# Optimization experiments

Measured on AMD Instinct MI355X. Metric: run time of the kernel, lower is better.

Reference implementation:

```python
import jax, jax.numpy as jnp
import numpy as np

NUM_BITS = 4
BLOCK = 64
OUT_F, IN_F = 4096, 4096
RANK = 16


def _uniform_table():
    # BlockQuantizer.create_uniform_map(symmetric=False, num_bits=4)
    return jnp.linspace(-1.0, 1.0, 2 ** NUM_BITS).astype(jnp.float32)


def _dequantize(qweight, weight_max):
    """Unpack 4-bit codes (2 per byte), lookup codebook, apply per-64 block scale.
    qweight: [OUT*IN/2, 1] int32 in [0,256); weight_max: [OUT*IN/64, 1] float32.
    Returns [OUT_F, IN_F] float32."""
    table = _uniform_table()
    q = qweight[:, 0]
    idx_lo = q & 15          # packed at shift 0
    idx_hi = (q >> 4) & 15   # packed at shift 4
    w = jnp.stack([table[idx_lo], table[idx_hi]], axis=-1)  # [N/2, 2]
    w = w.reshape(-1, BLOCK) * weight_max                   # per-block scale
    return w.reshape(OUT_F, IN_F)


def setup_inputs() -> dict:
    key = jax.random.key(0)
    k1, k2, k3, k4, k5, k6 = jax.random.split(key, 6)
    x = jax.random.normal(k1, (4, 2048, IN_F), dtype=jnp.float32)
    qweight = jax.random.randint(k2, (OUT_F * IN_F // 2, 1), 0, 256, dtype=jnp.int32)
    weight_max = jax.random.uniform(k3, (OUT_F * IN_F // BLOCK, 1), dtype=jnp.float32,
                                    minval=0.01, maxval=1.0)
    lora_A = jax.random.normal(k4, (RANK, IN_F), dtype=jnp.float32) * 0.02
    lora_B = jax.random.normal(k5, (OUT_F, RANK), dtype=jnp.float32) * 0.02
    bias = jax.random.normal(k6, (OUT_F,), dtype=jnp.float32) * 0.02
    return {"x": x, "qweight": qweight, "weight_max": weight_max,
            "lora_A": lora_A, "lora_B": lora_B, "bias": bias}


def reference(x, qweight, weight_max, lora_A, lora_B, bias):
    # Dequantize block-quantized base weight, then linear + LoRA correction.
    W = _dequantize(qweight, weight_max)                     # [out, in]
    y = jnp.einsum('bsi,oi->bso', x, W) + bias               # base linear
    a = jnp.einsum('bsi,ri->bsr', x, lora_A)                 # lora_A(x)
    y = y + jnp.einsum('bsr,or->bso', a, lora_B)             # + lora_B(.)
    return y
```

## Files before the change

### kernel.cpp

```cpp
#include <hip/hip_runtime.h>
#include <hip/hip_bf16.h>
#include <stdint.h>

typedef __bf16 bf16_t;
typedef bf16_t bf16x8 __attribute__((ext_vector_type(8)));
typedef float f32x4 __attribute__((ext_vector_type(4)));

#define IN_F 4096
#define OUT_F 4096
#define M_ROWS 8192
#define RANK 16

__global__ __launch_bounds__(256)
void dequant_lora_kernel(const int* __restrict__ qw, const float* __restrict__ wmax,
                         const float* __restrict__ lA, const float* __restrict__ lB,
                         bf16_t* __restrict__ Wp) {
  const int bid = blockIdx.x;
  const int bo = bid >> 4;
  const int bi = bid & 15;
  const int t  = threadIdx.x;
  const int o  = bo * 8 + (t >> 5);
  const int i0 = bi * 256 + (t & 31) * 8;
  const int f0 = o * IN_F + i0;

  const int4 q4 = *(const int4*)(qw + (f0 >> 1));
  const float scale = wmax[f0 >> 6];
  const float st = scale * (2.0f / 15.0f);

  float v[8];
  {
    const int q0 = q4.x, q1 = q4.y, q2 = q4.z, q3 = q4.w;
    v[0] = (float)(q0 & 15)        * st - scale;
    v[1] = (float)((q0 >> 4) & 15) * st - scale;
    v[2] = (float)(q1 & 15)        * st - scale;
    v[3] = (float)((q1 >> 4) & 15) * st - scale;
    v[4] = (float)(q2 & 15)        * st - scale;
    v[5] = (float)((q2 >> 4) & 15) * st - scale;
    v[6] = (float)(q3 & 15)        * st - scale;
    v[7] = (float)((q3 >> 4) & 15) * st - scale;
  }

  const float* Brow = lB + o * RANK;
#pragma unroll
  for (int r = 0; r < RANK; ++r) {
    const float br = Brow[r];
    const float4 a0 = *(const float4*)(lA + r * IN_F + i0);
    const float4 a1 = *(const float4*)(lA + r * IN_F + i0 + 4);
    v[0] += br * a0.x; v[1] += br * a0.y; v[2] += br * a0.z; v[3] += br * a0.w;
    v[4] += br * a1.x; v[5] += br * a1.y; v[6] += br * a1.z; v[7] += br * a1.w;
  }

  bf16x8 ov;
#pragma unroll
  for (int j = 0; j < 8; ++j) ov[j] = (bf16_t)v[j];
  *(bf16x8*)(Wp + (size_t)f0) = ov;
}

__global__ __launch_bounds__(256)
void f32_to_bf16_kernel(const float* __restrict__ x, bf16_t* __restrict__ xb) {
  const size_t tid = (size_t)blockIdx.x * 256 + threadIdx.x;
  const float4 a0 = *(const float4*)(x + tid * 8);
  const float4 a1 = *(const float4*)(x + tid * 8 + 4);
  bf16x8 o;
  o[0] = (bf16_t)a0.x; o[1] = (bf16_t)a0.y; o[2] = (bf16_t)a0.z; o[3] = (bf16_t)a0.w;
  o[4] = (bf16_t)a1.x; o[5] = (bf16_t)a1.y; o[6] = (bf16_t)a1.z; o[7] = (bf16_t)a1.w;
  *(bf16x8*)(xb + tid * 8) = o;
}

__device__ __forceinline__ void gld(const bf16_t* src, char* dst) {
  __builtin_amdgcn_global_load_lds((const __attribute__((address_space(1))) void*)src,
                                   (__attribute__((address_space(3))) void*)dst, 16, 0, 0);
}

#define BARRIER() __builtin_amdgcn_s_barrier()
#define WAIT_LGKM0() do { asm volatile("s_waitcnt lgkmcnt(0)" ::: "memory"); \
                          __builtin_amdgcn_sched_barrier(0); } while (0)
#define WAIT_VM(n) asm volatile("s_waitcnt vmcnt(" #n ")" ::: "memory")

#define LDA(buf, m, cb) (*(const bf16x8*)(ldsA + ((buf)*32768 + aRowB + (m)*2048 + (cb))))
#define LDB(buf, n, cb) (*(const bf16x8*)(ldsB + ((buf)*32768 + bRowB + (n)*2048 + (cb))))

#define STAGE_A(kt, buf) do { \
  _Pragma("unroll") for (int g = 0; g < 4; ++g) \
    gld(Asrc + ((size_t)g*64*IN_F + (size_t)(kt)*64), ldsA + ((buf)*32768 + g*8192 + tid*16)); \
} while (0)
#define STAGE_B_HALF(kt, buf, h) do { \
  _Pragma("unroll") for (int g = 0; g < 2; ++g) \
    gld(Bsrc + ((size_t)((h)*2+g)*64*IN_F + (size_t)(kt)*64), \
        ldsB + ((buf)*32768 + ((h)*2+g)*8192 + tid*16)); \
} while (0)
#define STAGE_B(kt, buf) do { STAGE_B_HALF(kt, buf, 0); STAGE_B_HALF(kt, buf, 1); } while (0)

#define READ_B_ALL(buf) do { \
  _Pragma("unroll") for (int n = 0; n < 4; ++n) { \
    b[n][0] = LDB(buf, n, cS0); b[n][1] = LDB(buf, n, cS1); } \
} while (0)

#define PHASE(Q, EXTRA, STAGE, TAILWAIT) do { \
  a[0][0] = LDA(cur, 2*(Q),   cS0); a[0][1] = LDA(cur, 2*(Q),   cS1); \
  a[1][0] = LDA(cur, 2*(Q)+1, cS0); a[1][1] = LDA(cur, 2*(Q)+1, cS1); \
  EXTRA; STAGE; \
  BARRIER(); \
  WAIT_LGKM0(); \
  __builtin_amdgcn_s_setprio(1); \
  _Pragma("unroll") for (int kh = 0; kh < 2; ++kh) \
    _Pragma("unroll") for (int mm = 0; mm < 2; ++mm) \
      _Pragma("unroll") for (int n = 0; n < 4; ++n) \
        acc[2*(Q)+mm][n] = __builtin_amdgcn_mfma_f32_16x16x32_bf16( \
            a[mm][kh], b[n][kh], acc[2*(Q)+mm][n], 0, 0, 0); \
  __builtin_amdgcn_s_setprio(0); \
  TAILWAIT; \
  BARRIER(); \
} while (0)

__global__ __launch_bounds__(512, 2)
void gemm_m201_kernel(const bf16_t* __restrict__ Xb, const bf16_t* __restrict__ Wp,
                      const float* __restrict__ bias, float* __restrict__ C) {
  __shared__ __align__(16) bf16_t As[2 * 16384];
  __shared__ __align__(16) bf16_t Bs[2 * 16384];
  char* ldsA = (char*)As;
  char* ldsB = (char*)Bs;

  const int tid  = threadIdx.x;
  const int lane = tid & 63;
  const int wave = tid >> 6;
  const int wr = wave >> 2;
  const int wc = wave & 3;
  const int r16 = lane & 15;
  const int kg  = lane >> 4;

  const int bid  = blockIdx.x;
  const int wgid = (bid & 7) * 64 + (bid >> 3);
  const int bm = wgid >> 4;
  const int bn = wgid & 15;

  const int srow = tid >> 3;
  const int scol = ((tid & 7) * 8) ^ (((tid >> 5) & 1) << 4);
  const bf16_t* Asrc = Xb + (size_t)(bm * 256 + srow) * IN_F + scol;
  const bf16_t* Bsrc = Wp + (size_t)(bn * 256 + srow) * IN_F + scol;

  const int aRowB = wr * 16384 + r16 * 128;
  const int bRowB = (wc >> 1) * 16384 + (wc & 1) * 8192 + r16 * 128;
  const int cS0 = (kg * 16) ^ ((r16 & 4) << 3);
  const int cS1 = cS0 + 64;

  f32x4 acc[8][4] = {};
  bf16x8 a[2][2], b[4][2];

  STAGE_A(0, 0); STAGE_B(0, 0);
  STAGE_A(1, 1); STAGE_B(1, 1);
  WAIT_VM(8);
  BARRIER();

  for (int t = 0; t < 64; ++t) {
    const int cur = t & 1;
    PHASE(0, READ_B_ALL(cur),
          { if (t >= 1 && t < 63) STAGE_A(t + 1, cur ^ 1); }, {});
    PHASE(1, {},
          { if (t < 62) STAGE_B_HALF(t + 2, cur, 0); }, {});
    PHASE(2, {},
          { if (t < 62) STAGE_B_HALF(t + 2, cur, 1); }, {});
    PHASE(3, {}, {},
          { if (t < 62) { WAIT_VM(4); } else if (t == 62) { WAIT_VM(0); } });
  }

#pragma unroll
  for (int n = 0; n < 4; ++n) {
    const int col = bn * 256 + wc * 64 + n * 16 + r16;
    const float bv = bias[col];
#pragma unroll
    for (int m = 0; m < 8; ++m) {
      const int row0 = bm * 256 + wr * 128 + m * 16 + kg * 4;
#pragma unroll
      for (int r = 0; r < 4; ++r)
        C[(size_t)(row0 + r) * OUT_F + col] = acc[m][n][r] + bv;
    }
  }
}

extern "C" void kernel_launch(void* const* d_in, const int* in_sizes, int n_in,
                              void* d_out, int out_size, void* d_ws, size_t ws_size,
                              hipStream_t stream) {
  const float* x  = (const float*)d_in[0];
  const int*   qw = (const int*)d_in[1];
  const float* wm = (const float*)d_in[2];
  const float* lA = (const float*)d_in[3];
  const float* lB = (const float*)d_in[4];
  const float* bs = (const float*)d_in[5];
  float* out = (float*)d_out;

  bf16_t* Wp = (bf16_t*)d_ws;
  bf16_t* Xb = (bf16_t*)((char*)d_ws + (size_t)OUT_F * IN_F * 2);

  dequant_lora_kernel<<<8192, 256, 0, stream>>>(qw, wm, lA, lB, Wp);
  f32_to_bf16_kernel<<<M_ROWS * IN_F / 8 / 256, 256, 0, stream>>>(x, Xb);
  gemm_m201_kernel<<<(M_ROWS / 256) * (OUT_F / 256), 512, 0, stream>>>(Xb, Wp, bs, out);
}
```

Before: 329.8 us.

## Fuse prep kernels and retile GEMM to 128x256 with K=32 for occupancy

Merges the dequant+LoRA and x-to-bf16 conversion kernels into one launch, split by block index. Retiles the GEMM from 256x256 tiles with K=64 to 128x256 tiles with K=32 per stage. This shrinks LDS use to 48 KB per workgroup and raises launch bounds to 4 waves per SIMD, so more workgroups can stay resident and hide latency. The trade-off is less data reuse per tile, more barriers per unit of work, and a simpler single-phase pipeline.

```diff
diff --git a/kernel.cpp b/kernel.cpp
--- a/kernel.cpp
+++ b/kernel.cpp
@@ -12,12 +12,23 @@
 #define RANK 16
 
 __global__ __launch_bounds__(256)
-void dequant_lora_kernel(const int* __restrict__ qw, const float* __restrict__ wmax,
-                         const float* __restrict__ lA, const float* __restrict__ lB,
-                         bf16_t* __restrict__ Wp) {
-  const int bid = blockIdx.x;
-  const int bo = bid >> 4;
-  const int bi = bid & 15;
+void prep_kernel(const float* __restrict__ x, const int* __restrict__ qw,
+                 const float* __restrict__ wmax, const float* __restrict__ lA,
+                 const float* __restrict__ lB, bf16_t* __restrict__ Wp,
+                 bf16_t* __restrict__ Xb) {
+  const int b = blockIdx.x;
+  if (b >= 8192) {
+    const size_t tid = (size_t)(b - 8192) * 256 + threadIdx.x;
+    const float4 a0 = *(const float4*)(x + tid * 8);
+    const float4 a1 = *(const float4*)(x + tid * 8 + 4);
+    bf16x8 o;
+    o[0] = (bf16_t)a0.x; o[1] = (bf16_t)a0.y; o[2] = (bf16_t)a0.z; o[3] = (bf16_t)a0.w;
+    o[4] = (bf16_t)a1.x; o[5] = (bf16_t)a1.y; o[6] = (bf16_t)a1.z; o[7] = (bf16_t)a1.w;
+    *(bf16x8*)(Xb + tid * 8) = o;
+    return;
+  }
+  const int bo = b >> 4;
+  const int bi = b & 15;
   const int t  = threadIdx.x;
   const int o  = bo * 8 + (t >> 5);
   const int i0 = bi * 256 + (t & 31) * 8;
@@ -56,17 +67,6 @@
   *(bf16x8*)(Wp + (size_t)f0) = ov;
 }
 
-__global__ __launch_bounds__(256)
-void f32_to_bf16_kernel(const float* __restrict__ x, bf16_t* __restrict__ xb) {
-  const size_t tid = (size_t)blockIdx.x * 256 + threadIdx.x;
-  const float4 a0 = *(const float4*)(x + tid * 8);
-  const float4 a1 = *(const float4*)(x + tid * 8 + 4);
-  bf16x8 o;
-  o[0] = (bf16_t)a0.x; o[1] = (bf16_t)a0.y; o[2] = (bf16_t)a0.z; o[3] = (bf16_t)a0.w;
-  o[4] = (bf16_t)a1.x; o[5] = (bf16_t)a1.y; o[6] = (bf16_t)a1.z; o[7] = (bf16_t)a1.w;
-  *(bf16x8*)(xb + tid * 8) = o;
-}
-
 __device__ __forceinline__ void gld(const bf16_t* src, char* dst) {
   __builtin_amdgcn_global_load_lds((const __attribute__((address_space(1))) void*)src,
                                    (__attribute__((address_space(3))) void*)dst, 16, 0, 0);
@@ -77,47 +77,35 @@
                           __builtin_amdgcn_sched_barrier(0); } while (0)
 #define WAIT_VM(n) asm volatile("s_waitcnt vmcnt(" #n ")" ::: "memory")
 
-#define LDA(buf, m, cb) (*(const bf16x8*)(ldsA + ((buf)*32768 + aRowB + (m)*2048 + (cb))))
-#define LDB(buf, n, cb) (*(const bf16x8*)(ldsB + ((buf)*32768 + bRowB + (n)*2048 + (cb))))
-
-#define STAGE_A(kt, buf) do { \
-  _Pragma("unroll") for (int g = 0; g < 4; ++g) \
-    gld(Asrc + ((size_t)g*64*IN_F + (size_t)(kt)*64), ldsA + ((buf)*32768 + g*8192 + tid*16)); \
-} while (0)
-#define STAGE_B_HALF(kt, buf, h) do { \
-  _Pragma("unroll") for (int g = 0; g < 2; ++g) \
-    gld(Bsrc + ((size_t)((h)*2+g)*64*IN_F + (size_t)(kt)*64), \
-        ldsB + ((buf)*32768 + ((h)*2+g)*8192 + tid*16)); \
-} while (0)
-#define STAGE_B(kt, buf) do { STAGE_B_HALF(kt, buf, 0); STAGE_B_HALF(kt, buf, 1); } while (0)
-
-#define READ_B_ALL(buf) do { \
-  _Pragma("unroll") for (int n = 0; n < 4; ++n) { \
-    b[n][0] = LDB(buf, n, cS0); b[n][1] = LDB(buf, n, cS1); } \
+#define STAGE(kt, buf) do { \
+  gld(Asrc + (size_t)(kt) * 32,                      ldsA + (buf)*8192  + tid*16); \
+  gld(Bsrc + (size_t)(kt) * 32,                      ldsB + (buf)*16384 + tid*16); \
+  gld(Bsrc + (size_t)128*IN_F + (size_t)(kt) * 32,   ldsB + (buf)*16384 + 8192 + tid*16); \
 } while (0)
 
-#define PHASE(Q, EXTRA, STAGE, TAILWAIT) do { \
-  a[0][0] = LDA(cur, 2*(Q),   cS0); a[0][1] = LDA(cur, 2*(Q),   cS1); \
-  a[1][0] = LDA(cur, 2*(Q)+1, cS0); a[1][1] = LDA(cur, 2*(Q)+1, cS1); \
-  EXTRA; STAGE; \
+#define LDAf(buf, m) (*(const bf16x8*)(ldsA + (buf)*8192  + aRowB + (m)*1024 + cSw))
+#define LDBf(buf, n) (*(const bf16x8*)(ldsB + (buf)*16384 + bRowB + (n)*1024 + cSw))
+
+#define TILE(CUR, STG, TW) do { \
+  _Pragma("unroll") for (int m = 0; m < 4; ++m) a[m] = LDAf(CUR, m); \
+  _Pragma("unroll") for (int n = 0; n < 4; ++n) b[n] = LDBf(CUR, n); \
+  WAIT_LGKM0(); \
   BARRIER(); \
-  WAIT_LGKM0(); \
+  STG; \
   __builtin_amdgcn_s_setprio(1); \
-  _Pragma("unroll") for (int kh = 0; kh < 2; ++kh) \
-    _Pragma("unroll") for (int mm = 0; mm < 2; ++mm) \
-      _Pragma("unroll") for (int n = 0; n < 4; ++n) \
-        acc[2*(Q)+mm][n] = __builtin_amdgcn_mfma_f32_16x16x32_bf16( \
-            a[mm][kh], b[n][kh], acc[2*(Q)+mm][n], 0, 0, 0); \
+  _Pragma("unroll") for (int m = 0; m < 4; ++m) \
+  _Pragma("unroll") for (int n = 0; n < 4; ++n) \
+    acc[m][n] = __builtin_amdgcn_mfma_f32_16x16x32_bf16(a[m], b[n], acc[m][n], 0, 0, 0); \
   __builtin_amdgcn_s_setprio(0); \
-  TAILWAIT; \
+  TW; \
   BARRIER(); \
 } while (0)
 
-__global__ __launch_bounds__(512, 2)
-void gemm_m201_kernel(const bf16_t* __restrict__ Xb, const bf16_t* __restrict__ Wp,
+__global__ __launch_bounds__(512, 4)
+void gemm_occ2_kernel(const bf16_t* __restrict__ Xb, const bf16_t* __restrict__ Wp,
                       const float* __restrict__ bias, float* __restrict__ C) {
-  __shared__ __align__(16) bf16_t As[2 * 16384];
-  __shared__ __align__(16) bf16_t Bs[2 * 16384];
+  __shared__ __align__(16) bf16_t As[2 * 4096];
+  __shared__ __align__(16) bf16_t Bs[2 * 8192];
   char* ldsA = (char*)As;
   char* ldsB = (char*)Bs;
 
@@ -130,47 +118,43 @@
   const int kg  = lane >> 4;
 
   const int bid  = blockIdx.x;
-  const int wgid = (bid & 7) * 64 + (bid >> 3);
+  const int wgid = (bid & 7) * 128 + (bid >> 3);
   const int bm = wgid >> 4;
   const int bn = wgid & 15;
 
-  const int srow = tid >> 3;
-  const int scol = ((tid & 7) * 8) ^ (((tid >> 5) & 1) << 4);
-  const bf16_t* Asrc = Xb + (size_t)(bm * 256 + srow) * IN_F + scol;
-  const bf16_t* Bsrc = Wp + (size_t)(bn * 256 + srow) * IN_F + scol;
+  const int srow = tid >> 2;
+  const int ss   = (tid & 3) ^ ((tid >> 3) & 3);
+  const bf16_t* Asrc = Xb + (size_t)(bm * 128 + srow) * IN_F + ss * 8;
+  const bf16_t* Bsrc = Wp + (size_t)(bn * 256 + srow) * IN_F + ss * 8;
 
-  const int aRowB = wr * 16384 + r16 * 128;
-  const int bRowB = (wc >> 1) * 16384 + (wc & 1) * 8192 + r16 * 128;
-  const int cS0 = (kg * 16) ^ ((r16 & 4) << 3);
-  const int cS1 = cS0 + 64;
+  const int cSw   = (kg ^ ((r16 >> 1) & 3)) * 16;
+  const int aRowB = (wr * 64 + r16) * 64;
+  const int bRowB = (wc * 64 + r16) * 64;
 
-  f32x4 acc[8][4] = {};
-  bf16x8 a[2][2], b[4][2];
+  f32x4 acc[4][4] = {};
+  bf16x8 a[4], b[4];
 
-  STAGE_A(0, 0); STAGE_B(0, 0);
-  STAGE_A(1, 1); STAGE_B(1, 1);
-  WAIT_VM(8);
+  STAGE(0, 0);
+  STAGE(1, 1);
+  WAIT_VM(3);
   BARRIER();
 
-  for (int t = 0; t < 64; ++t) {
-    const int cur = t & 1;
-    PHASE(0, READ_B_ALL(cur),
-          { if (t >= 1 && t < 63) STAGE_A(t + 1, cur ^ 1); }, {});
-    PHASE(1, {},
-          { if (t < 62) STAGE_B_HALF(t + 2, cur, 0); }, {});
-    PHASE(2, {},
-          { if (t < 62) STAGE_B_HALF(t + 2, cur, 1); }, {});
-    PHASE(3, {}, {},
-          { if (t < 62) { WAIT_VM(4); } else if (t == 62) { WAIT_VM(0); } });
+  for (int tt = 0; tt < 124; tt += 2) {
+    TILE(0, STAGE(tt + 2, 0), WAIT_VM(3));
+    TILE(1, STAGE(tt + 3, 1), WAIT_VM(3));
   }
+  TILE(0, STAGE(126, 0), WAIT_VM(3));
+  TILE(1, STAGE(127, 1), WAIT_VM(3));
+  TILE(0, {},            WAIT_VM(0));
+  TILE(1, {},            {});
 
 #pragma unroll
   for (int n = 0; n < 4; ++n) {
     const int col = bn * 256 + wc * 64 + n * 16 + r16;
     const float bv = bias[col];
 #pragma unroll
-    for (int m = 0; m < 8; ++m) {
-      const int row0 = bm * 256 + wr * 128 + m * 16 + kg * 4;
+    for (int m = 0; m < 4; ++m) {
+      const int row0 = bm * 128 + wr * 64 + m * 16 + kg * 4;
 #pragma unroll
       for (int r = 0; r < 4; ++r)
         C[(size_t)(row0 + r) * OUT_F + col] = acc[m][n][r] + bv;
@@ -192,7 +176,6 @@
   bf16_t* Wp = (bf16_t*)d_ws;
   bf16_t* Xb = (bf16_t*)((char*)d_ws + (size_t)OUT_F * IN_F * 2);
 
-  dequant_lora_kernel<<<8192, 256, 0, stream>>>(qw, wm, lA, lB, Wp);
-  f32_to_bf16_kernel<<<M_ROWS * IN_F / 8 / 256, 256, 0, stream>>>(x, Xb);
-  gemm_m201_kernel<<<(M_ROWS / 256) * (OUT_F / 256), 512, 0, stream>>>(Xb, Wp, bs, out);
+  prep_kernel<<<24576, 256, 0, stream>>>(x, qw, wm, lA, lB, Wp, Xb);
+  gemm_occ2_kernel<<<(M_ROWS / 128) * (OUT_F / 256), 512, 0, stream>>>(Xb, Wp, bs, out);
 }
```

New measurement: 334.5 us. About the same (+1.4%).

## Switch GEMM to 32x32x16 MFMA with new LDS swizzle and fuse prep kernels

Applied to the files above, without the earlier changes.

Replaces the 16x16x32 bf16 MFMA inner loop with 32x32x16 MFMA tiles, which changes the per-wave fragment layout, the LDS XOR swizzle and the epilogue row mapping. The larger instruction needs fewer LDS fragment reads per FLOP. It also merges the dequant+LoRA kernel and the x-to-bf16 conversion into one launch, saving a kernel launch and the gap between them. The risk is new LDS bank conflicts from the different swizzle and a more scattered epilogue store pattern.

```diff
diff --git a/kernel.cpp b/kernel.cpp
--- a/kernel.cpp
+++ b/kernel.cpp
@@ -5,6 +5,7 @@
 typedef __bf16 bf16_t;
 typedef bf16_t bf16x8 __attribute__((ext_vector_type(8)));
 typedef float f32x4 __attribute__((ext_vector_type(4)));
+typedef float f32x16 __attribute__((ext_vector_type(16)));
 
 #define IN_F 4096
 #define OUT_F 4096
@@ -12,12 +13,23 @@
 #define RANK 16
 
 __global__ __launch_bounds__(256)
-void dequant_lora_kernel(const int* __restrict__ qw, const float* __restrict__ wmax,
-                         const float* __restrict__ lA, const float* __restrict__ lB,
-                         bf16_t* __restrict__ Wp) {
-  const int bid = blockIdx.x;
-  const int bo = bid >> 4;
-  const int bi = bid & 15;
+void prep_kernel(const float* __restrict__ x, const int* __restrict__ qw,
+                 const float* __restrict__ wmax, const float* __restrict__ lA,
+                 const float* __restrict__ lB, bf16_t* __restrict__ Wp,
+                 bf16_t* __restrict__ Xb) {
+  const int b = blockIdx.x;
+  if (b >= 8192) {
+    const size_t tid = (size_t)(b - 8192) * 256 + threadIdx.x;
+    const float4 a0 = *(const float4*)(x + tid * 8);
+    const float4 a1 = *(const float4*)(x + tid * 8 + 4);
+    bf16x8 o;
+    o[0] = (bf16_t)a0.x; o[1] = (bf16_t)a0.y; o[2] = (bf16_t)a0.z; o[3] = (bf16_t)a0.w;
+    o[4] = (bf16_t)a1.x; o[5] = (bf16_t)a1.y; o[6] = (bf16_t)a1.z; o[7] = (bf16_t)a1.w;
+    *(bf16x8*)(Xb + tid * 8) = o;
+    return;
+  }
+  const int bo = b >> 4;
+  const int bi = b & 15;
   const int t  = threadIdx.x;
   const int o  = bo * 8 + (t >> 5);
   const int i0 = bi * 256 + (t & 31) * 8;
@@ -56,17 +68,6 @@
   *(bf16x8*)(Wp + (size_t)f0) = ov;
 }
 
-__global__ __launch_bounds__(256)
-void f32_to_bf16_kernel(const float* __restrict__ x, bf16_t* __restrict__ xb) {
-  const size_t tid = (size_t)blockIdx.x * 256 + threadIdx.x;
-  const float4 a0 = *(const float4*)(x + tid * 8);
-  const float4 a1 = *(const float4*)(x + tid * 8 + 4);
-  bf16x8 o;
-  o[0] = (bf16_t)a0.x; o[1] = (bf16_t)a0.y; o[2] = (bf16_t)a0.z; o[3] = (bf16_t)a0.w;
-  o[4] = (bf16_t)a1.x; o[5] = (bf16_t)a1.y; o[6] = (bf16_t)a1.z; o[7] = (bf16_t)a1.w;
-  *(bf16x8*)(xb + tid * 8) = o;
-}
-
 __device__ __forceinline__ void gld(const bf16_t* src, char* dst) {
   __builtin_amdgcn_global_load_lds((const __attribute__((address_space(1))) void*)src,
                                    (__attribute__((address_space(3))) void*)dst, 16, 0, 0);
@@ -77,9 +78,6 @@
                           __builtin_amdgcn_sched_barrier(0); } while (0)
 #define WAIT_VM(n) asm volatile("s_waitcnt vmcnt(" #n ")" ::: "memory")
 
-#define LDA(buf, m, cb) (*(const bf16x8*)(ldsA + ((buf)*32768 + aRowB + (m)*2048 + (cb))))
-#define LDB(buf, n, cb) (*(const bf16x8*)(ldsB + ((buf)*32768 + bRowB + (n)*2048 + (cb))))
-
 #define STAGE_A(kt, buf) do { \
   _Pragma("unroll") for (int g = 0; g < 4; ++g) \
     gld(Asrc + ((size_t)g*64*IN_F + (size_t)(kt)*64), ldsA + ((buf)*32768 + g*8192 + tid*16)); \
@@ -91,31 +89,35 @@
 } while (0)
 #define STAGE_B(kt, buf) do { STAGE_B_HALF(kt, buf, 0); STAGE_B_HALF(kt, buf, 1); } while (0)
 
+#define LDA32(buf, P, c) (*(const bf16x8*)(ldsA + ((buf)*32768 + aBase + (P)*4096 + cc##c)))
+#define LDB32(buf, nt, c) (*(const bf16x8*)(ldsB + ((buf)*32768 + bBase + (nt)*4096 + cc##c)))
+
 #define READ_B_ALL(buf) do { \
-  _Pragma("unroll") for (int n = 0; n < 4; ++n) { \
-    b[n][0] = LDB(buf, n, cS0); b[n][1] = LDB(buf, n, cS1); } \
-} while (0)
-
-#define PHASE(Q, EXTRA, STAGE, TAILWAIT) do { \
-  a[0][0] = LDA(cur, 2*(Q),   cS0); a[0][1] = LDA(cur, 2*(Q),   cS1); \
-  a[1][0] = LDA(cur, 2*(Q)+1, cS0); a[1][1] = LDA(cur, 2*(Q)+1, cS1); \
+  bT[0][0] = LDB32(buf, 0, 0); bT[0][1] = LDB32(buf, 0, 1); \
+  bT[0][2] = LDB32(buf, 0, 2); bT[0][3] = LDB32(buf, 0, 3); \
+  bT[1][0] = LDB32(buf, 1, 0); bT[1][1] = LDB32(buf, 1, 1); \
+  bT[1][2] = LDB32(buf, 1, 2); bT[1][3] = LDB32(buf, 1, 3); \
+} while (0)
+
+#define PHASE(P, EXTRA, STAGE, TAILWAIT) do { \
+  aF[0] = LDA32(cur, P, 0); aF[1] = LDA32(cur, P, 1); \
+  aF[2] = LDA32(cur, P, 2); aF[3] = LDA32(cur, P, 3); \
   EXTRA; STAGE; \
   BARRIER(); \
   WAIT_LGKM0(); \
   __builtin_amdgcn_s_setprio(1); \
-  _Pragma("unroll") for (int kh = 0; kh < 2; ++kh) \
-    _Pragma("unroll") for (int mm = 0; mm < 2; ++mm) \
-      _Pragma("unroll") for (int n = 0; n < 4; ++n) \
-        acc[2*(Q)+mm][n] = __builtin_amdgcn_mfma_f32_16x16x32_bf16( \
-            a[mm][kh], b[n][kh], acc[2*(Q)+mm][n], 0, 0, 0); \
+  _Pragma("unroll") for (int c = 0; c < 4; ++c) \
+    _Pragma("unroll") for (int nt = 0; nt < 2; ++nt) \
+      acc[P][nt] = __builtin_amdgcn_mfma_f32_32x32x16_bf16( \
+          aF[c], bT[nt][c], acc[P][nt], 0, 0, 0); \
   __builtin_amdgcn_s_setprio(0); \
   TAILWAIT; \
   BARRIER(); \
 } while (0)
 
 __global__ __launch_bounds__(512, 2)
-void gemm_m201_kernel(const bf16_t* __restrict__ Xb, const bf16_t* __restrict__ Wp,
-                      const float* __restrict__ bias, float* __restrict__ C) {
+void gemm_32x32_kernel(const bf16_t* __restrict__ Xb, const bf16_t* __restrict__ Wp,
+                       const float* __restrict__ bias, float* __restrict__ C) {
   __shared__ __align__(16) bf16_t As[2 * 16384];
   __shared__ __align__(16) bf16_t Bs[2 * 16384];
   char* ldsA = (char*)As;
@@ -126,8 +128,8 @@
   const int wave = tid >> 6;
   const int wr = wave >> 2;
   const int wc = wave & 3;
-  const int r16 = lane & 15;
-  const int kg  = lane >> 4;
+  const int l31 = lane & 31;
+  const int kg2 = lane >> 5;
 
   const int bid  = blockIdx.x;
   const int wgid = (bid & 7) * 64 + (bid >> 3);
@@ -135,17 +137,20 @@
   const int bn = wgid & 15;
 
   const int srow = tid >> 3;
-  const int scol = ((tid & 7) * 8) ^ (((tid >> 5) & 1) << 4);
+  const int scol = ((tid & 7) ^ (srow & 7)) * 8;
   const bf16_t* Asrc = Xb + (size_t)(bm * 256 + srow) * IN_F + scol;
   const bf16_t* Bsrc = Wp + (size_t)(bn * 256 + srow) * IN_F + scol;
 
-  const int aRowB = wr * 16384 + r16 * 128;
-  const int bRowB = (wc >> 1) * 16384 + (wc & 1) * 8192 + r16 * 128;
-  const int cS0 = (kg * 16) ^ ((r16 & 4) << 3);
-  const int cS1 = cS0 + 64;
-
-  f32x4 acc[8][4] = {};
-  bf16x8 a[2][2], b[4][2];
+  const int aBase = wr * 16384 + l31 * 128;
+  const int bBase = wc * 8192  + l31 * 128;
+  const int xr  = (lane & 7) * 16;
+  const int cc0 = (0  | kg2 * 16) ^ xr;
+  const int cc1 = (32 | kg2 * 16) ^ xr;
+  const int cc2 = (64 | kg2 * 16) ^ xr;
+  const int cc3 = (96 | kg2 * 16) ^ xr;
+
+  f32x16 acc[4][2] = {};
+  bf16x8 aF[4], bT[2][4];
 
   STAGE_A(0, 0); STAGE_B(0, 0);
   STAGE_A(1, 1); STAGE_B(1, 1);
@@ -165,15 +170,17 @@
   }
 
 #pragma unroll
-  for (int n = 0; n < 4; ++n) {
-    const int col = bn * 256 + wc * 64 + n * 16 + r16;
+  for (int nt = 0; nt < 2; ++nt) {
+    const int col = bn * 256 + wc * 64 + nt * 32 + l31;
     const float bv = bias[col];
 #pragma unroll
-    for (int m = 0; m < 8; ++m) {
-      const int row0 = bm * 256 + wr * 128 + m * 16 + kg * 4;
-#pragma unroll
-      for (int r = 0; r < 4; ++r)
-        C[(size_t)(row0 + r) * OUT_F + col] = acc[m][n][r] + bv;
+    for (int mt = 0; mt < 4; ++mt) {
+      const int rowbase = bm * 256 + wr * 128 + mt * 32 + kg2 * 4;
+#pragma unroll
+      for (int reg = 0; reg < 16; ++reg) {
+        const int row = rowbase + (reg & 3) + 8 * (reg >> 2);
+        C[(size_t)row * OUT_F + col] = acc[mt][nt][reg] + bv;
+      }
     }
   }
 }
@@ -192,7 +199,6 @@
   bf16_t* Wp = (bf16_t*)d_ws;
   bf16_t* Xb = (bf16_t*)((char*)d_ws + (size_t)OUT_F * IN_F * 2);
 
-  dequant_lora_kernel<<<8192, 256, 0, stream>>>(qw, wm, lA, lB, Wp);
-  f32_to_bf16_kernel<<<M_ROWS * IN_F / 8 / 256, 256, 0, stream>>>(x, Xb);
-  gemm_m201_kernel<<<(M_ROWS / 256) * (OUT_F / 256), 512, 0, stream>>>(Xb, Wp, bs, out);
-}
+  prep_kernel<<<24576, 256, 0, stream>>>(x, qw, wm, lA, lB, Wp, Xb);
+  gemm_32x32_kernel<<<(M_ROWS / 256) * (OUT_F / 256), 512, 0, stream>>>(Xb, Wp, bs, out);
+}
```

Result: slower. 338.3 us (+2.6%).
